# Performance work log

Measured on AMD Instinct MI355X. Metric: run time of the kernel, lower is better.

The kernel has to match this reference:

```python
import jax, jax.numpy as jnp
import numpy as np

EMBED_DIM = 1024
NUM_HEADS = 16
HEAD_DIM = EMBED_DIM // NUM_HEADS
SCALE = HEAD_DIM ** -0.5


def setup_inputs() -> dict:
    key = jax.random.key(0)
    k1, k2, k3 = jax.random.split(key, 3)
    B, S, E = 2, 2048, EMBED_DIM
    # xavier-uniform-like init scaled down for stability
    x = jax.random.normal(k1, (B, S, E), dtype=jnp.float32)
    w_qkv = jax.random.normal(k2, (3 * E, E), dtype=jnp.float32) * (E ** -0.5)
    w_out = jax.random.normal(k3, (E, E), dtype=jnp.float32) * (E ** -0.5)
    bias_qkv = jnp.zeros((3 * E,), dtype=jnp.float32)
    bias_out = jnp.zeros((E,), dtype=jnp.float32)
    return {"x": x, "w_qkv": w_qkv, "bias_qkv": bias_qkv, "w_out": w_out, "bias_out": bias_out}


def reference(x, w_qkv, bias_qkv, w_out, bias_out):
    B, S, E = x.shape
    H, D = NUM_HEADS, HEAD_DIM
    # fused QKV projection: nn.Linear semantics -> x @ w_qkv.T + bias
    qkv = jnp.einsum('bse,fe->bsf', x, w_qkv) + bias_qkv  # [B,S,3E]
    q, k, v = jnp.split(qkv, 3, axis=-1)
    # reshape to heads
    q = q.reshape(B, S, H, D)
    k = k.reshape(B, S, H, D)
    v = v.reshape(B, S, H, D)
    # scaled dot-product attention (non-causal)
    scores = jnp.einsum('bqhd,bkhd->bhqk', q, k) * SCALE  # [B,H,S,S]
    probs = jax.nn.softmax(scores, axis=-1)
    ctx = jnp.einsum('bhqk,bkhd->bqhd', probs, v).reshape(B, S, E)
    # output projection
    out = jnp.einsum('bse,fe->bsf', ctx, w_out) + bias_out
    return out
```

## Files before the change

### kernel.cpp

```cpp
#include <hip/hip_runtime.h>
#include <hip/hip_bf16.h>


typedef __bf16 bf16_t;
typedef __bf16 bf16x4 __attribute__((ext_vector_type(4)));
typedef __bf16 bf16x8 __attribute__((ext_vector_type(8)));
typedef float f32x4 __attribute__((ext_vector_type(4)));

#define MFMA16(a, b, c) __builtin_amdgcn_mfma_f32_16x16x32_bf16(a, b, c, 0, 0, 0)

static constexpr int Bn = 2;
static constexpr int S = 2048;
static constexpr int E = 1024;
static constexpr int H = 16;
static constexpr int Dh = 64;

__device__ __forceinline__ void gl_lds16(const bf16_t* g, bf16_t* l) {
  __builtin_amdgcn_global_load_lds(
      (const __attribute__((address_space(1))) unsigned int*)g,
      (__attribute__((address_space(3))) unsigned int*)l, 16, 0, 0);
}

__device__ __forceinline__ int detect_fp32(const unsigned short* p) {
  int cnt = 0;
#pragma unroll
  for (int j = 0; j < 32; j++) {
    const int e = (p[j] >> 7) & 0xFF;
    cnt += (e > 140) ? 1 : 0;
  }
  return cnt >= 2;
}

static constexpr int G0 = 4194304 / 8;
static constexpr int G1 = G0 + 3145728 / 8;
static constexpr int G2 = G1 + 3072 / 8;
static constexpr int G3 = G2 + 1048576 / 8;
static constexpr int G4 = G3 + 1024 / 8;

__global__ void convert_all(const void* __restrict__ s0, const void* __restrict__ s1,
                            const void* __restrict__ s2, const void* __restrict__ s3,
                            const void* __restrict__ s4, bf16_t* __restrict__ dst) {
  const int fp32 = detect_fp32((const unsigned short*)s0);
  const int stride = gridDim.x * blockDim.x;
  for (int i = blockIdx.x * blockDim.x + threadIdx.x; i < G4; i += stride) {
    const void* s;
    int off;
    if (i < G0)      { s = s0; off = i; }
    else if (i < G1) { s = s1; off = i - G0; }
    else if (i < G2) { s = s2; off = i - G1; }
    else if (i < G3) { s = s3; off = i - G2; }
    else             { s = s4; off = i - G3; }
    bf16x8 o;
    if (fp32) {
      const float* sp = (const float*)s + off * 8;
#pragma unroll
      for (int j = 0; j < 8; j++) o[j] = (bf16_t)sp[j];
    } else {
      o = *((const bf16x8*)s + off);
    }
    *(bf16x8*)(dst + (size_t)i * 8) = o;
  }
}

__global__ __launch_bounds__(256) void gemm_qkv(
    const bf16_t* __restrict__ X, const bf16_t* __restrict__ W,
    const bf16_t* __restrict__ bias,
    bf16_t* __restrict__ Qo, bf16_t* __restrict__ Ko, bf16_t* __restrict__ Vo) {
  __shared__ bf16_t Alds[16 * 512];
  __shared__ bf16_t Blds[16 * 512];
  const int tid = threadIdx.x;
  const int wave = tid >> 6, lane = tid & 63;
  const int lr = lane & 15, quad = lane >> 4;
  const int wm = wave >> 1, wn = wave & 1;
  const int m0 = blockIdx.y * 128, n0 = blockIdx.x * 128;
  constexpr int Kd = 1024;

  f32x4 acc[4][4] = {};
  for (int k0 = 0; k0 < Kd; k0 += 64) {
    __syncthreads();
#pragma unroll
    for (int i = 0; i < 4; i++) {
      const int fb = wave * 4 + i;
      const int mt = fb >> 1, kc = fb & 1;
      gl_lds16(X + (size_t)(m0 + mt * 16 + lr) * Kd + k0 + kc * 32 + quad * 8,
               &Alds[fb * 512]);
      gl_lds16(W + (size_t)(n0 + mt * 16 + lr) * Kd + k0 + kc * 32 + quad * 8,
               &Blds[fb * 512]);
    }
    __syncthreads();
#pragma unroll
    for (int kc = 0; kc < 2; kc++) {
      bf16x8 af[4], bfr[4];
#pragma unroll
      for (int mt = 0; mt < 4; mt++)
        af[mt] = *(const bf16x8*)&Alds[((wm * 4 + mt) * 2 + kc) * 512 + lane * 8];
#pragma unroll
      for (int nt = 0; nt < 4; nt++)
        bfr[nt] = *(const bf16x8*)&Blds[((wn * 4 + nt) * 2 + kc) * 512 + lane * 8];
#pragma unroll
      for (int mt = 0; mt < 4; mt++)
#pragma unroll
        for (int nt = 0; nt < 4; nt++)
          acc[mt][nt] = MFMA16(af[mt], bfr[nt], acc[mt][nt]);
    }
  }

  const int m0w = m0 + wm * 64, n0w = n0 + wn * 64;
#pragma unroll
  for (int nt = 0; nt < 4; nt++) {
    const int col = n0w + nt * 16 + lr;
    const float bs = (float)bias[col];
    const int which = col >> 10;
    const int e = col & 1023;
    const int h = e >> 6, d = e & 63;
#pragma unroll
    for (int mt = 0; mt < 4; mt++) {
      const int row0 = m0w + mt * 16 + quad * 4;
      const int b = row0 >> 11, s0 = row0 & 2047;
      if (which == 2) {
        bf16x4 v4;
#pragma unroll
        for (int r = 0; r < 4; r++) v4[r] = (bf16_t)(acc[mt][nt][r] + bs);
        *(bf16x4*)&Vo[((size_t)((b * H + h) * Dh + d)) * S + s0] = v4;
      } else {
        bf16_t* dst = (which == 0) ? Qo : Ko;
#pragma unroll
        for (int r = 0; r < 4; r++)
          dst[((size_t)((b * H + h) * S + (s0 + r))) * Dh + d] =
              (bf16_t)(acc[mt][nt][r] + bs);
      }
    }
  }
}

__global__ __launch_bounds__(256, 4) void attn_kernel(
    const bf16_t* __restrict__ Q, const bf16_t* __restrict__ K,
    const bf16_t* __restrict__ Vt, bf16_t* __restrict__ CTX) {
  constexpr int LDP = 72;
  __shared__ bf16_t Kl[8 * 512];
  __shared__ bf16_t Vl[8 * 512];
  __shared__ bf16_t Psh[4 * 16 * LDP];

  const int tid = threadIdx.x;
  const int wave = tid >> 6, lane = tid & 63;
  const int lr = lane & 15, quad = lane >> 4;

  const int blk = blockIdx.x;
  const int bh = blk & 31;
  const int qt = blk >> 5;
  const int b = bh >> 4, h = bh & 15;

  const bf16_t* Qb = Q + (size_t)bh * S * Dh;
  const bf16_t* Kb = K + (size_t)bh * S * Dh;
  const bf16_t* Vb = Vt + (size_t)bh * Dh * S;

  const int q0 = qt * 64 + wave * 16;

  const bf16x8 aq0 = *(const bf16x8*)(Qb + (size_t)(q0 + lr) * Dh + quad * 8);
  const bf16x8 aq1 = *(const bf16x8*)(Qb + (size_t)(q0 + lr) * Dh + 32 + quad * 8);

  bf16x8 ones;
#pragma unroll
  for (int j = 0; j < 8; j++) ones[j] = (bf16_t)1.0f;

  bf16_t* pw = &Psh[wave * 16 * LDP];

  const bf16_t* kg = Kb + (size_t)(wave * 16 + lr) * Dh + quad * 8;
  const bf16_t* vg = Vb + (size_t)(wave * 16 + lr) * S + quad * 8;

  f32x4 O[4] = {};
  f32x4 lacc = {};

  for (int sk0 = 0; sk0 < S; sk0 += 64) {
    __syncthreads();
    gl_lds16(kg + (size_t)sk0 * Dh, &Kl[(wave * 2 + 0) * 512]);
    gl_lds16(kg + (size_t)sk0 * Dh + 32, &Kl[(wave * 2 + 1) * 512]);
    gl_lds16(vg + sk0, &Vl[(wave * 2 + 0) * 512]);
    gl_lds16(vg + sk0 + 32, &Vl[(wave * 2 + 1) * 512]);
    __syncthreads();

    f32x4 sc[4];
#pragma unroll
    for (int nt = 0; nt < 4; nt++) {
      const bf16x8 k0f = *(const bf16x8*)&Kl[(nt * 2 + 0) * 512 + lane * 8];
      const bf16x8 k1f = *(const bf16x8*)&Kl[(nt * 2 + 1) * 512 + lane * 8];
      f32x4 z = {};
      z = MFMA16(aq0, k0f, z);
      sc[nt] = MFMA16(aq1, k1f, z);
    }

    bf16x8 vf[4][2];
#pragma unroll
    for (int dt = 0; dt < 4; dt++) {
      vf[dt][0] = *(const bf16x8*)&Vl[(dt * 2 + 0) * 512 + lane * 8];
      vf[dt][1] = *(const bf16x8*)&Vl[(dt * 2 + 1) * 512 + lane * 8];
    }

#pragma unroll
    for (int nt = 0; nt < 4; nt++)
#pragma unroll
      for (int r = 0; r < 4; r++) {
        const float p = __expf(sc[nt][r] * 0.125f);
        pw[(quad * 4 + r) * LDP + nt * 16 + lr] = (bf16_t)p;
      }

    const bf16x8 ap0 = *(const bf16x8*)(&pw[lr * LDP + quad * 8]);
    const bf16x8 ap1 = *(const bf16x8*)(&pw[lr * LDP + 32 + quad * 8]);
    lacc = MFMA16(ap0, ones, lacc);
    lacc = MFMA16(ap1, ones, lacc);
#pragma unroll
    for (int dt = 0; dt < 4; dt++) {
      O[dt] = MFMA16(ap0, vf[dt][0], O[dt]);
      O[dt] = MFMA16(ap1, vf[dt][1], O[dt]);
    }
  }

  float rl[4];
#pragma unroll
  for (int r = 0; r < 4; r++) rl[r] = 1.0f / lacc[r];
#pragma unroll
  for (int dt = 0; dt < 4; dt++)
#pragma unroll
    for (int r = 0; r < 4; r++) {
      const int qrow = q0 + quad * 4 + r;
      CTX[(size_t)(b * S + qrow) * E + h * 64 + dt * 16 + lr] =
          (bf16_t)(O[dt][r] * rl[r]);
    }
}

__global__ __launch_bounds__(256) void gemm_out(
    const bf16_t* __restrict__ X, const bf16_t* __restrict__ W,
    const bf16_t* __restrict__ bias, void* __restrict__ Out,
    const void* __restrict__ xin) {
  __shared__ bf16_t Alds[8 * 512];
  __shared__ bf16_t Blds[16 * 512];
  const int tid = threadIdx.x;
  const int wave = tid >> 6, lane = tid & 63;
  const int lr = lane & 15, quad = lane >> 4;
  const int wm = wave >> 1, wn = wave & 1;
  const int m0 = blockIdx.y * 64, n0 = blockIdx.x * 128;
  constexpr int Kd = 1024;

  f32x4 acc[2][4] = {};
  for (int k0 = 0; k0 < Kd; k0 += 64) {
    __syncthreads();
#pragma unroll
    for (int kc = 0; kc < 2; kc++)
      gl_lds16(X + (size_t)(m0 + wave * 16 + lr) * Kd + k0 + kc * 32 + quad * 8,
               &Alds[(wave * 2 + kc) * 512]);
#pragma unroll
    for (int i = 0; i < 2; i++) {
      const int nt = wave * 2 + i;
#pragma unroll
      for (int kc = 0; kc < 2; kc++)
        gl_lds16(W + (size_t)(n0 + nt * 16 + lr) * Kd + k0 + kc * 32 + quad * 8,
                 &Blds[(nt * 2 + kc) * 512]);
    }
    __syncthreads();
#pragma unroll
    for (int kc = 0; kc < 2; kc++) {
      bf16x8 af[2], bfr[4];
#pragma unroll
      for (int mt = 0; mt < 2; mt++)
        af[mt] = *(const bf16x8*)&Alds[((wm * 2 + mt) * 2 + kc) * 512 + lane * 8];
#pragma unroll
      for (int nt = 0; nt < 4; nt++)
        bfr[nt] = *(const bf16x8*)&Blds[((wn * 4 + nt) * 2 + kc) * 512 + lane * 8];
#pragma unroll
      for (int mt = 0; mt < 2; mt++)
#pragma unroll
        for (int nt = 0; nt < 4; nt++)
          acc[mt][nt] = MFMA16(af[mt], bfr[nt], acc[mt][nt]);
    }
  }

  const int fp32 = detect_fp32((const unsigned short*)xin);
  const int m0w = m0 + wm * 32, n0w = n0 + wn * 64;
#pragma unroll
  for (int nt = 0; nt < 4; nt++) {
    const int col = n0w + nt * 16 + lr;
    const float bs = (float)bias[col];
#pragma unroll
    for (int mt = 0; mt < 2; mt++) {
#pragma unroll
      for (int r = 0; r < 4; r++) {
        const int row = m0w + mt * 16 + quad * 4 + r;
        const float v = acc[mt][nt][r] + bs;
        if (fp32)
          ((float*)Out)[(size_t)row * E + col] = v;
        else
          ((bf16_t*)Out)[(size_t)row * E + col] = (bf16_t)v;
      }
    }
  }
}

extern "C" void kernel_launch(void* const* d_in, const int* in_sizes, int n_in,
                              void* d_out, int out_size, void* d_ws, size_t ws_size,
                              hipStream_t stream) {
  const void* x = d_in[0];
  const void* w_qkv = d_in[1];
  const void* b_qkv = d_in[2];
  const void* w_out = d_in[3];
  const void* b_out = d_in[4];

  bf16_t* base = (bf16_t*)d_ws;
  const int N_X = Bn * S * E;
  const int N_WQ = 3 * E * E;
  const int N_BQ = 3 * E;
  const int N_WO = E * E;
  const int N_BO = E;
  bf16_t* xb = base;
  bf16_t* wqb = xb + N_X;
  bf16_t* bqb = wqb + N_WQ;
  bf16_t* wob = bqb + N_BQ;
  bf16_t* bob = wob + N_WO;
  const size_t QKV_ELEMS = (size_t)Bn * H * S * Dh;
  bf16_t* Qw = bob + N_BO;
  bf16_t* Kw = Qw + QKV_ELEMS;
  bf16_t* Vw = Kw + QKV_ELEMS;
  bf16_t* CTXw = Vw + QKV_ELEMS;

  convert_all<<<1024, 256, 0, stream>>>(x, w_qkv, b_qkv, w_out, b_out, xb);
  gemm_qkv<<<dim3(3 * E / 128, Bn * S / 128), 256, 0, stream>>>(xb, wqb, bqb, Qw, Kw, Vw);
  attn_kernel<<<32 * Bn * H, 256, 0, stream>>>(Qw, Kw, Vw, CTXw);
  gemm_out<<<dim3(E / 128, Bn * S / 64), 256, 0, stream>>>(CTXw, wob, bob, d_out, x);
}
```

Baseline: 228.7 us.

## Keep attention probabilities in registers via transposed score MFMA

The score MFMA now computes S^T, with K as operand A and Q as operand B, so each lane's exponentiated probabilities already sit in the B-operand layout of a 16x16x16 bf16 MFMA. This removes the per-tile LDS round trip for P and the ones-vector MFMA used for the row sums. The sums are now accumulated in scalar registers and reduced with two cross-lane shuffles at the end, and the output is written as packed 4-element vectors. In exchange it issues more, smaller MFMAs (K=16 instead of K=32) for P·V, and V is read from LDS in 4-element chunks.

New measurement: 229.3 us. About the same (+0.3%).

```diff
diff --git a/kernel.cpp b/kernel.cpp
--- a/kernel.cpp
+++ b/kernel.cpp
@@ -5,9 +5,11 @@
 typedef __bf16 bf16_t;
 typedef __bf16 bf16x4 __attribute__((ext_vector_type(4)));
 typedef __bf16 bf16x8 __attribute__((ext_vector_type(8)));
+typedef short s16x4 __attribute__((ext_vector_type(4)));
 typedef float f32x4 __attribute__((ext_vector_type(4)));
 
 #define MFMA16(a, b, c) __builtin_amdgcn_mfma_f32_16x16x32_bf16(a, b, c, 0, 0, 0)
+#define MFMA16X16(a, b, c) __builtin_amdgcn_mfma_f32_16x16x16bf16_1k(a, b, c, 0, 0, 0)
 
 static constexpr int Bn = 2;
 static constexpr int S = 2048;
@@ -136,10 +138,8 @@
 __global__ __launch_bounds__(256, 4) void attn_kernel(
     const bf16_t* __restrict__ Q, const bf16_t* __restrict__ K,
     const bf16_t* __restrict__ Vt, bf16_t* __restrict__ CTX) {
-  constexpr int LDP = 72;
   __shared__ bf16_t Kl[8 * 512];
   __shared__ bf16_t Vl[8 * 512];
-  __shared__ bf16_t Psh[4 * 16 * LDP];
 
   const int tid = threadIdx.x;
   const int wave = tid >> 6, lane = tid & 63;
@@ -159,17 +159,13 @@
   const bf16x8 aq0 = *(const bf16x8*)(Qb + (size_t)(q0 + lr) * Dh + quad * 8);
   const bf16x8 aq1 = *(const bf16x8*)(Qb + (size_t)(q0 + lr) * Dh + 32 + quad * 8);
 
-  bf16x8 ones;
-#pragma unroll
-  for (int j = 0; j < 8; j++) ones[j] = (bf16_t)1.0f;
-
-  bf16_t* pw = &Psh[wave * 16 * LDP];
-
   const bf16_t* kg = Kb + (size_t)(wave * 16 + lr) * Dh + quad * 8;
   const bf16_t* vg = Vb + (size_t)(wave * 16 + lr) * S + quad * 8;
 
+  const int vq = ((quad >> 1) * 16 + lr) * 8 + (quad & 1) * 4;
+
   f32x4 O[4] = {};
-  f32x4 lacc = {};
+  float lp = 0.f;
 
   for (int sk0 = 0; sk0 < S; sk0 += 64) {
     __syncthreads();
@@ -179,53 +175,46 @@
     gl_lds16(vg + sk0 + 32, &Vl[(wave * 2 + 1) * 512]);
     __syncthreads();
 
-    f32x4 sc[4];
-#pragma unroll
-    for (int nt = 0; nt < 4; nt++) {
-      const bf16x8 k0f = *(const bf16x8*)&Kl[(nt * 2 + 0) * 512 + lane * 8];
-      const bf16x8 k1f = *(const bf16x8*)&Kl[(nt * 2 + 1) * 512 + lane * 8];
+#pragma unroll
+    for (int kt = 0; kt < 4; kt++) {
+      const bf16x8 kf0 = *(const bf16x8*)&Kl[(kt * 2 + 0) * 512 + lane * 8];
+      const bf16x8 kf1 = *(const bf16x8*)&Kl[(kt * 2 + 1) * 512 + lane * 8];
       f32x4 z = {};
-      z = MFMA16(aq0, k0f, z);
-      sc[nt] = MFMA16(aq1, k1f, z);
-    }
-
-    bf16x8 vf[4][2];
-#pragma unroll
-    for (int dt = 0; dt < 4; dt++) {
-      vf[dt][0] = *(const bf16x8*)&Vl[(dt * 2 + 0) * 512 + lane * 8];
-      vf[dt][1] = *(const bf16x8*)&Vl[(dt * 2 + 1) * 512 + lane * 8];
-    }
-
-#pragma unroll
-    for (int nt = 0; nt < 4; nt++)
+      z = MFMA16(kf0, aq0, z);
+      const f32x4 sc = MFMA16(kf1, aq1, z);
+
+      bf16x4 pb;
+      float ps = 0.f;
 #pragma unroll
       for (int r = 0; r < 4; r++) {
-        const float p = __expf(sc[nt][r] * 0.125f);
-        pw[(quad * 4 + r) * LDP + nt * 16 + lr] = (bf16_t)p;
+        const float p = __expf(sc[r] * 0.125f);
+        ps += p;
+        pb[r] = (bf16_t)p;
       }
-
-    const bf16x8 ap0 = *(const bf16x8*)(&pw[lr * LDP + quad * 8]);
-    const bf16x8 ap1 = *(const bf16x8*)(&pw[lr * LDP + 32 + quad * 8]);
-    lacc = MFMA16(ap0, ones, lacc);
-    lacc = MFMA16(ap1, ones, lacc);
-#pragma unroll
-    for (int dt = 0; dt < 4; dt++) {
-      O[dt] = MFMA16(ap0, vf[dt][0], O[dt]);
-      O[dt] = MFMA16(ap1, vf[dt][1], O[dt]);
-    }
-  }
-
-  float rl[4];
-#pragma unroll
-  for (int r = 0; r < 4; r++) rl[r] = 1.0f / lacc[r];
-#pragma unroll
-  for (int dt = 0; dt < 4; dt++)
-#pragma unroll
-    for (int r = 0; r < 4; r++) {
-      const int qrow = q0 + quad * 4 + r;
-      CTX[(size_t)(b * S + qrow) * E + h * 64 + dt * 16 + lr] =
-          (bf16_t)(O[dt][r] * rl[r]);
-    }
+      lp += ps;
+      const s16x4 pbi = __builtin_bit_cast(s16x4, pb);
+
+      const int vbase = (kt >> 1) * 512 + ((kt & 1) * 256 + vq);
+#pragma unroll
+      for (int dt = 0; dt < 4; dt++) {
+        const bf16x4 va = *(const bf16x4*)&Vl[dt * 1024 + vbase];
+        O[dt] = MFMA16X16(__builtin_bit_cast(s16x4, va), pbi, O[dt]);
+      }
+    }
+  }
+
+  lp += __shfl_xor(lp, 16);
+  lp += __shfl_xor(lp, 32);
+  const float rl = 1.0f / lp;
+
+  const int qrow = q0 + lr;
+#pragma unroll
+  for (int dt = 0; dt < 4; dt++) {
+    bf16x4 o4;
+#pragma unroll
+    for (int r = 0; r < 4; r++) o4[r] = (bf16_t)(O[dt][r] * rl);
+    *(bf16x4*)&CTX[(size_t)(b * S + qrow) * E + h * 64 + dt * 16 + quad * 4] = o4;
+  }
 }
 
 __global__ __launch_bounds__(256) void gemm_out(
```
